# Kernel optimization log

Hardware: AMD Instinct MI355X
Metric: run time of the kernel (lower is better)

The kernel has to match this reference:

```python
import jax, jax.numpy as jnp
import numpy as np

B, T, DIN, H = 32, 4096, 256, 256


def _log_g(x):
    # log of g(x) = where(x>=0, x+0.5, sigmoid(x)), computed stably in log space
    return jnp.where(x >= 0.0, jnp.log(jax.nn.relu(x) + 0.5), -jax.nn.softplus(-x))


def setup_inputs() -> dict:
    key = jax.random.key(0)
    ks = jax.random.split(key, 4)
    scale = (6.0 / (DIN + H)) ** 0.5  # xavier_uniform
    return {
        "x": jax.random.normal(ks[0], (B, T, DIN), dtype=jnp.float32),
        "h0": jax.random.normal(ks[1], (B, 1, H), dtype=jnp.float32),
        "Wz": jax.random.uniform(ks[2], (H, DIN), jnp.float32, -scale, scale),
        "bz": jnp.zeros((H,), jnp.float32),
        "Wh": jax.random.uniform(ks[3], (H, DIN), jnp.float32, -scale, scale),
        "bh": jnp.zeros((H,), jnp.float32),
    }


def reference(x, h0, Wz, bz, Wh, bh):
    # minGRU training path: log-space parallel scan (Heinsen scan)
    k = jnp.einsum("bti,hi->bth", x, Wz) + bz            # pre-activation of z gate
    log_z = -jax.nn.softplus(-k)                           # log sigmoid(k)
    log_coeffs = -jax.nn.softplus(k)                       # log(1 - sigmoid(k))
    log_h0 = _log_g(h0)                                    # (B,1,H)
    log_tilde_h = _log_g(jnp.einsum("bti,hi->bth", x, Wh) + bh)
    log_values = jnp.concatenate([log_h0, log_z + log_tilde_h], axis=1)  # (B,T+1,H)
    # a_star[t] = sum_{s<=t} log_coeffs[s], with a leading zero
    a_star = jnp.cumsum(jnp.pad(log_coeffs, ((0, 0), (1, 0), (0, 0))), axis=1)
    # logcumsumexp along time via associative scan with logaddexp
    lcse = jax.lax.associative_scan(jnp.logaddexp, log_values - a_star, axis=1)
    log_h = a_star + lcse                                  # (B,T+1,H)
    return jnp.exp(log_h[:, 1:])                           # (B,T,H)
```

## Files before the change

### kernel.cpp

```cpp
#include <hip/hip_runtime.h>
#include <hip/hip_fp16.h>

typedef __attribute__((ext_vector_type(8))) short short8;
typedef __attribute__((ext_vector_type(4))) float f32x4;
typedef unsigned short ushort_t;
typedef unsigned int uint_t;

#define B_SZ 32
#define T_SZ 4096
#define D_IN 256
#define H_SZ 256
#define M_SZ (B_SZ * T_SZ)
#define CHUNK 64
#define NCHUNK (T_SZ / CHUNK)

__device__ __forceinline__ ushort_t f2bf(float f) {
  unsigned int u = __float_as_uint(f);
  unsigned int r = (u + 0x7FFFu + ((u >> 16) & 1u)) >> 16;
  return (ushort_t)r;
}

__device__ __forceinline__ float sigmoidf_(float xv) {
  float e = __expf(-fabsf(xv));
  float s = 1.0f / (1.0f + e);
  return xv >= 0.0f ? s : 1.0f - s;
}

__device__ __forceinline__ float unpack_lo(uint_t pk) {
  return __half2float(__ushort_as_half((ushort_t)(pk & 0xFFFFu)));
}
__device__ __forceinline__ float unpack_hi(uint_t pk) {
  return __half2float(__ushort_as_half((ushort_t)(pk >> 16)));
}

__global__ void prep_w(const float* __restrict__ Wz, const float* __restrict__ Wh,
                       ushort_t* __restrict__ wsB) {
  int g = blockIdx.x * 256 + threadIdx.x;
  if (g >= 8 * 2048) return;
  int ks = g >> 11;
  int r = g & 2047;
  int c = r >> 9;
  int n = r & 511;
  int h = (n >> 5) * 16 + (n & 15);
  const float* W = ((n >> 4) & 1) ? Wh : Wz;
  const float* src = W + (size_t)h * D_IN + ks * 32 + c * 8;
  ushort_t* dst = wsB + (size_t)g * 8;
#pragma unroll
  for (int j = 0; j < 8; ++j) dst[j] = f2bf(src[j]);
}

__global__ __launch_bounds__(512, 4) void gemm_av(
    const float* __restrict__ x, const ushort_t* __restrict__ wsB,
    const float* __restrict__ bz, const float* __restrict__ bh,
    uint_t* __restrict__ av, float2* cAV) {
  __shared__ __align__(16) unsigned char lds[73728];
  ushort_t* As = (ushort_t*)lds;
  ushort_t* Bs = (ushort_t*)(lds + 8192);

  const int tid = threadIdx.x;
  const int lane = tid & 63;
  const int wid = tid >> 6;
  const int m0 = blockIdx.x * 64;

  const int a_row = (tid >> 1) & 63;
  const int a_c = tid >> 7;
  const int a_half = tid & 1;
  const float* asrc = x + (size_t)(m0 + a_row) * D_IN + a_c * 8 + a_half * 4;

  float4 pf[8];
#pragma unroll
  for (int ks = 0; ks < 8; ++ks) pf[ks] = *(const float4*)(asrc + ks * 32);

  f32x4 acc[4][4];
#pragma unroll
  for (int rt = 0; rt < 4; ++rt)
#pragma unroll
    for (int ct = 0; ct < 4; ++ct) {
      f32x4 z4 = {0.f, 0.f, 0.f, 0.f};
      acc[rt][ct] = z4;
    }

  {
    const ushort_t* bsrc = wsB + (size_t)wid * 2048 + lane * 8;
    ushort_t* bdst = Bs + wid * 2048;
#pragma unroll
    for (int cc = 0; cc < 4; ++cc) {
      __builtin_amdgcn_global_load_lds(
          (const __attribute__((address_space(1))) void*)(bsrc + cc * 512),
          (__attribute__((address_space(3))) void*)(bdst + cc * 512), 16, 0, 0);
    }
    uint2 w;
    w.x = (uint_t)f2bf(pf[0].x) | ((uint_t)f2bf(pf[0].y) << 16);
    w.y = (uint_t)f2bf(pf[0].z) | ((uint_t)f2bf(pf[0].w) << 16);
    *(uint2*)((char*)As + tid * 8) = w;
  }
  __syncthreads();

#pragma unroll
  for (int ks = 0; ks < 8; ++ks) {
    const int cur = ks & 1;
    short8 afr[4], bfr[4];
    {
      const int c = lane >> 4;
      const int r16 = lane & 15;
#pragma unroll
      for (int rt = 0; rt < 4; ++rt) {
        int row = rt * 16 + r16;
        afr[rt] = *(const short8*)(As + cur * 2048 + (c * 64 + row) * 8);
      }
#pragma unroll
      for (int ct = 0; ct < 4; ++ct) {
        int n = wid * 64 + ct * 16 + r16;
        bfr[ct] = *(const short8*)(Bs + cur * 16384 + (c * 512 + n) * 8);
      }
    }
    if (ks < 7) {
      const ushort_t* bsrc = wsB + (size_t)(ks + 1) * 16384 + wid * 2048 + lane * 8;
      ushort_t* bdst = Bs + (cur ^ 1) * 16384 + wid * 2048;
#pragma unroll
      for (int cc = 0; cc < 4; ++cc) {
        __builtin_amdgcn_global_load_lds(
            (const __attribute__((address_space(1))) void*)(bsrc + cc * 512),
            (__attribute__((address_space(3))) void*)(bdst + cc * 512), 16, 0, 0);
      }
    }
#pragma unroll
    for (int rt = 0; rt < 4; ++rt)
#pragma unroll
      for (int ct = 0; ct < 4; ++ct)
        acc[rt][ct] = __builtin_amdgcn_mfma_f32_16x16x32_bf16(
            afr[rt], bfr[ct], acc[rt][ct], 0, 0, 0);
    if (ks < 7) {
      uint2 w;
      w.x = (uint_t)f2bf(pf[ks + 1].x) | ((uint_t)f2bf(pf[ks + 1].y) << 16);
      w.y = (uint_t)f2bf(pf[ks + 1].z) | ((uint_t)f2bf(pf[ks + 1].w) << 16);
      *(uint2*)((char*)As + (cur ^ 1) * 4096 + tid * 8) = w;
    }
    __syncthreads();
  }

  const int col16 = lane & 15;
  const int rgrp = lane >> 4;
#pragma unroll
  for (int i = 0; i < 2; ++i) {
    int hh = (wid * 2 + i) * 16 + col16;
    float bzv = bz[hh];
    float bhv = bh[hh];
    float CA = 1.0f, CV = 0.0f;
#pragma unroll
    for (int rt = 0; rt < 4; ++rt) {
      float A4 = 1.0f, V4 = 0.0f;
#pragma unroll
      for (int j = 0; j < 4; ++j) {
        int row = m0 + rt * 16 + rgrp * 4 + j;
        float kv = acc[rt][2 * i][j] + bzv;
        float pv = acc[rt][2 * i + 1][j] + bhv;
        float a = sigmoidf_(-kv);
        float z = 1.0f - a;
        float gg = (pv >= 0.0f) ? (pv + 0.5f) : sigmoidf_(pv);
        float vv = z * gg;
        uint_t pk = (uint_t)__half_as_ushort(__float2half_rn(a)) |
                    ((uint_t)__half_as_ushort(__float2half_rn(vv)) << 16);
        av[(size_t)row * H_SZ + hh] = pk;
        V4 = fmaf(a, V4, vv);
        A4 *= a;
      }
      float Ap = __shfl_xor(A4, 16);
      float Vp = __shfl_xor(V4, 16);
      float A8 = A4 * Ap;
      float V8 = (lane & 16) ? fmaf(A4, Vp, V4) : fmaf(Ap, V4, Vp);
      float Ap2 = __shfl_xor(A8, 32);
      float Vp2 = __shfl_xor(V8, 32);
      float A16 = A8 * Ap2;
      float V16 = (lane & 32) ? fmaf(A8, Vp2, V8) : fmaf(Ap2, V8, Vp2);
      CV = fmaf(A16, CV, V16);
      CA = CA * A16;
    }
    if (cAV != nullptr && lane < 16) {
      float2 r; r.x = CA; r.y = CV;
      cAV[(size_t)blockIdx.x * H_SZ + hh] = r;
    }
  }
}

__global__ __launch_bounds__(256) void chunk_carry(
    const float* __restrict__ h0, const float2* __restrict__ cAV,
    float* __restrict__ hb) {
  const int b = blockIdx.x;
  const int h = threadIdx.x;
  float v0 = h0[b * H_SZ + h];
  float hc = (v0 >= 0.0f) ? (v0 + 0.5f) : sigmoidf_(v0);

  const float2* p = cAV + (size_t)b * NCHUNK * H_SZ + h;
  float* o = hb + (size_t)b * NCHUNK * H_SZ + h;

  float2 buf[NCHUNK];
#pragma unroll
  for (int c = 0; c < NCHUNK; ++c) buf[c] = p[(size_t)c * H_SZ];

#pragma unroll
  for (int c = 0; c < NCHUNK; ++c) {
    o[(size_t)c * H_SZ] = hc;
    hc = fmaf(buf[c].x, hc, buf[c].y);
  }
}

__global__ __launch_bounds__(256) void chunk_scan_out(
    const uint_t* av, const float* __restrict__ hb, float* out) {
  const int b = blockIdx.x >> 6;
  const int c = blockIdx.x & 63;
  const int h = threadIdx.x;

  float hc = hb[((size_t)b * NCHUNK + c) * H_SZ + h];
  const uint_t* p = av + ((size_t)b * T_SZ + c * CHUNK) * H_SZ + h;
  float* o = out + ((size_t)b * T_SZ + c * CHUNK) * H_SZ + h;

  uint_t buf[CHUNK];
#pragma unroll
  for (int s = 0; s < CHUNK; ++s) buf[s] = p[(size_t)s * H_SZ];

#pragma unroll
  for (int s = 0; s < CHUNK; ++s) {
    float a = unpack_lo(buf[s]);
    float v = unpack_hi(buf[s]);
    hc = fmaf(a, hc, v);
    o[(size_t)s * H_SZ] = hc;
  }
}

__global__ __launch_bounds__(64) void scan_seq(const float* __restrict__ h0,
                                               const uint_t* av, float* out) {
  const int b = blockIdx.x >> 2;
  const int hg = blockIdx.x & 3;
  const int h = hg * 64 + threadIdx.x;

  float v0 = h0[b * H_SZ + h];
  float hc = (v0 >= 0.0f) ? (v0 + 0.5f) : sigmoidf_(v0);

  const uint_t* p = av + (size_t)b * T_SZ * H_SZ + h;
  float* o = out + (size_t)b * T_SZ * H_SZ + h;

  uint_t buf[32];
#pragma unroll
  for (int d = 0; d < 32; ++d) buf[d] = p[(size_t)d * H_SZ];

  for (int t0 = 0; t0 < T_SZ; t0 += 32) {
#pragma unroll
    for (int d = 0; d < 32; ++d) {
      int t = t0 + d;
      uint_t pk = buf[d];
      int tn = t + 32;
      if (tn < T_SZ) buf[d] = p[(size_t)tn * H_SZ];
      hc = fmaf(unpack_lo(pk), hc, unpack_hi(pk));
      o[(size_t)t * H_SZ] = hc;
    }
  }
}

extern "C" void kernel_launch(void* const* d_in, const int* in_sizes, int n_in,
                              void* d_out, int out_size, void* d_ws, size_t ws_size,
                              hipStream_t stream) {
  const float* x  = (const float*)d_in[0];
  const float* h0 = (const float*)d_in[1];
  const float* Wz = (const float*)d_in[2];
  const float* bz = (const float*)d_in[3];
  const float* Wh = (const float*)d_in[4];
  const float* bh = (const float*)d_in[5];
  float* out = (float*)d_out;

  const size_t wsBBytes = 262144;
  const size_t cavBytes = (size_t)B_SZ * NCHUNK * H_SZ * 8;
  const size_t hbBytes  = (size_t)B_SZ * NCHUNK * H_SZ * 4;
  const size_t avOff    = 8388608;
  const size_t avBytes  = (size_t)M_SZ * H_SZ * 4;

  ushort_t* wsB = (ushort_t*)d_ws;
  float2* cAV = (float2*)((char*)d_ws + wsBBytes);
  float* hb   = (float*)((char*)d_ws + wsBBytes + cavBytes);

  const bool haveSummaries = ws_size >= wsBBytes + cavBytes + hbBytes;
  uint_t* av;
  if (ws_size >= avOff + avBytes) {
    av = (uint_t*)((char*)d_ws + avOff);
  } else {
    av = (uint_t*)d_out;
  }

  prep_w<<<64, 256, 0, stream>>>(Wz, Wh, wsB);
  gemm_av<<<M_SZ / 64, 512, 0, stream>>>(x, wsB, bz, bh, av,
                                         haveSummaries ? cAV : (float2*)nullptr);
  if (haveSummaries) {
    chunk_carry<<<B_SZ, 256, 0, stream>>>(h0, cAV, hb);
    chunk_scan_out<<<B_SZ * NCHUNK, 256, 0, stream>>>(av, hb, out);
  } else {
    scan_seq<<<B_SZ * 4, 64, 0, stream>>>(h0, av, out);
  }
}
```

Before: 166.0 us.

## Triple-buffer B tiles with prefetch depth two and explicit vmcnt waits

Moves the weight-tile staging to three LDS buffers, issuing global-to-LDS loads two k-steps ahead, and replaces __syncthreads with partial s_waitcnt vmcnt(4) plus raw barriers so later loads stay in flight. B loads are issued before the x prefetch. LDS grows to about 104 KB and launch bounds drop to 1 block per CU, which can reduce occupancy and latency hiding across blocks. The manual vmcnt count depends on the exact order of issued memory ops, so a miscount could cause a race.

```diff
diff --git a/kernel.cpp b/kernel.cpp
--- a/kernel.cpp
+++ b/kernel.cpp
@@ -49,11 +49,11 @@
   for (int j = 0; j < 8; ++j) dst[j] = f2bf(src[j]);
 }
 
-__global__ __launch_bounds__(512, 4) void gemm_av(
+__global__ __launch_bounds__(512, 1) void gemm_av(
     const float* __restrict__ x, const ushort_t* __restrict__ wsB,
     const float* __restrict__ bz, const float* __restrict__ bh,
     uint_t* __restrict__ av, float2* cAV) {
-  __shared__ __align__(16) unsigned char lds[73728];
+  __shared__ __align__(16) unsigned char lds[106496];
   ushort_t* As = (ushort_t*)lds;
   ushort_t* Bs = (ushort_t*)(lds + 8192);
 
@@ -67,28 +67,35 @@
   const int a_half = tid & 1;
   const float* asrc = x + (size_t)(m0 + a_row) * D_IN + a_c * 8 + a_half * 4;
 
-  float4 pf[8];
-#pragma unroll
-  for (int ks = 0; ks < 8; ++ks) pf[ks] = *(const float4*)(asrc + ks * 32);
-
-  f32x4 acc[4][4];
-#pragma unroll
-  for (int rt = 0; rt < 4; ++rt)
-#pragma unroll
-    for (int ct = 0; ct < 4; ++ct) {
-      f32x4 z4 = {0.f, 0.f, 0.f, 0.f};
-      acc[rt][ct] = z4;
-    }
-
-  {
-    const ushort_t* bsrc = wsB + (size_t)wid * 2048 + lane * 8;
-    ushort_t* bdst = Bs + wid * 2048;
+  auto STAGE_B = [&](int ks, int buf) {
+    const ushort_t* bsrc = wsB + (size_t)ks * 16384 + wid * 2048 + lane * 8;
+    ushort_t* bdst = Bs + buf * 16384 + wid * 2048;
 #pragma unroll
     for (int cc = 0; cc < 4; ++cc) {
       __builtin_amdgcn_global_load_lds(
           (const __attribute__((address_space(1))) void*)(bsrc + cc * 512),
           (__attribute__((address_space(3))) void*)(bdst + cc * 512), 16, 0, 0);
     }
+  };
+
+  STAGE_B(0, 0);
+  STAGE_B(1, 1);
+
+  float4 pf[8];
+#pragma unroll
+  for (int ks = 0; ks < 8; ++ks) pf[ks] = *(const float4*)(asrc + ks * 32);
+  asm volatile("" ::: "memory");
+
+  f32x4 acc[4][4];
+#pragma unroll
+  for (int rt = 0; rt < 4; ++rt)
+#pragma unroll
+    for (int ct = 0; ct < 4; ++ct) {
+      f32x4 z4 = {0.f, 0.f, 0.f, 0.f};
+      acc[rt][ct] = z4;
+    }
+
+  {
     uint2 w;
     w.x = (uint_t)f2bf(pf[0].x) | ((uint_t)f2bf(pf[0].y) << 16);
     w.y = (uint_t)f2bf(pf[0].z) | ((uint_t)f2bf(pf[0].w) << 16);
@@ -98,7 +105,8 @@
 
 #pragma unroll
   for (int ks = 0; ks < 8; ++ks) {
-    const int cur = ks & 1;
+    const int rbuf = ks % 3;
+    const int acur = ks & 1;
     short8 afr[4], bfr[4];
     {
       const int c = lane >> 4;
@@ -106,24 +114,15 @@
 #pragma unroll
       for (int rt = 0; rt < 4; ++rt) {
         int row = rt * 16 + r16;
-        afr[rt] = *(const short8*)(As + cur * 2048 + (c * 64 + row) * 8);
+        afr[rt] = *(const short8*)(As + acur * 2048 + (c * 64 + row) * 8);
       }
 #pragma unroll
       for (int ct = 0; ct < 4; ++ct) {
         int n = wid * 64 + ct * 16 + r16;
-        bfr[ct] = *(const short8*)(Bs + cur * 16384 + (c * 512 + n) * 8);
+        bfr[ct] = *(const short8*)(Bs + rbuf * 16384 + (c * 512 + n) * 8);
       }
     }
-    if (ks < 7) {
-      const ushort_t* bsrc = wsB + (size_t)(ks + 1) * 16384 + wid * 2048 + lane * 8;
-      ushort_t* bdst = Bs + (cur ^ 1) * 16384 + wid * 2048;
-#pragma unroll
-      for (int cc = 0; cc < 4; ++cc) {
-        __builtin_amdgcn_global_load_lds(
-            (const __attribute__((address_space(1))) void*)(bsrc + cc * 512),
-            (__attribute__((address_space(3))) void*)(bdst + cc * 512), 16, 0, 0);
-      }
-    }
+    if (ks < 6) STAGE_B(ks + 2, (ks + 2) % 3);
 #pragma unroll
     for (int rt = 0; rt < 4; ++rt)
 #pragma unroll
@@ -134,9 +133,17 @@
       uint2 w;
       w.x = (uint_t)f2bf(pf[ks + 1].x) | ((uint_t)f2bf(pf[ks + 1].y) << 16);
       w.y = (uint_t)f2bf(pf[ks + 1].z) | ((uint_t)f2bf(pf[ks + 1].w) << 16);
-      *(uint2*)((char*)As + (cur ^ 1) * 4096 + tid * 8) = w;
-    }
-    __syncthreads();
+      *(uint2*)((char*)As + (acur ^ 1) * 4096 + tid * 8) = w;
+    }
+    if (ks < 7) {
+      if (ks < 6) {
+        asm volatile("s_waitcnt vmcnt(4) lgkmcnt(0)" ::: "memory");
+      } else {
+        asm volatile("s_waitcnt vmcnt(0) lgkmcnt(0)" ::: "memory");
+      }
+      __builtin_amdgcn_s_barrier();
+      __builtin_amdgcn_sched_barrier(0);
+    }
   }
 
   const int col16 = lane & 15;
```

After: 191.8 us. 1.16x slower.
